# Kernel tuning notes

Measured on AMD Instinct MI355X. Metric: run time of the kernel, lower is better.

The kernel has to match this reference:

```python
import jax, jax.numpy as jnp
import numpy as np

D_NODE = 100
D_HID = 300
EPS = 1e-5


def _gru_step_h0(x, W_ih, b_ih, b_hh):
    # Single torch-GRU step with h0 = 0 (seq len 1), so W_hh @ h0 vanishes
    # and only the hidden biases b_hh survive.
    gi = x @ W_ih.T + b_ih                      # [..., 3*H]
    H = D_HID
    r = jax.nn.sigmoid(gi[..., 0:H] + b_hh[0:H])
    z = jax.nn.sigmoid(gi[..., H:2 * H] + b_hh[H:2 * H])
    n = jnp.tanh(gi[..., 2 * H:3 * H] + r * b_hh[2 * H:3 * H])
    return (1.0 - z) * n                        # h' = (1-z)*n + z*0


def setup_inputs() -> dict:
    key = jax.random.key(0)
    ks = jax.random.split(key, 20)
    B, T, Lq, N = 128, 512, 256, 256
    s = 0.02
    inp = {
        "nodes": jax.random.normal(ks[0], (B * N, D_NODE), jnp.float32),
        "context_rep": jax.random.normal(ks[1], (B, Lq, D_HID), jnp.float32),
        "dia_triples": jax.random.randint(ks[2], (B, T, 3), 0, N, jnp.int64 if jax.config.jax_enable_x64 else jnp.int32),
        "node_number": N,
        # mean_trans: Linear(100, 300)
        "W_mean": s * jax.random.normal(ks[3], (D_HID, D_NODE), jnp.float32),
        "b_mean": jnp.zeros((D_HID,), jnp.float32),
        # bidirectional GRU(300 -> 300); h0=0 so W_hh drops out, keep biases
        "W_ih_f": s * jax.random.normal(ks[4], (3 * D_HID, D_HID), jnp.float32),
        "b_ih_f": s * jax.random.normal(ks[5], (3 * D_HID,), jnp.float32),
        "b_hh_f": s * jax.random.normal(ks[6], (3 * D_HID,), jnp.float32),
        "W_ih_b": s * jax.random.normal(ks[7], (3 * D_HID, D_HID), jnp.float32),
        "b_ih_b": s * jax.random.normal(ks[8], (3 * D_HID,), jnp.float32),
        "b_hh_b": s * jax.random.normal(ks[9], (3 * D_HID,), jnp.float32),
        # output_trans: Linear(600, 300) + tanh
        "W_out": s * jax.random.normal(ks[10], (D_HID, 2 * D_HID), jnp.float32),
        "b_out": jnp.zeros((D_HID,), jnp.float32),
        # trans_node_to_decoder_dim: Linear(100, 300)
        "W_node": s * jax.random.normal(ks[11], (D_HID, D_NODE), jnp.float32),
        "b_node": jnp.zeros((D_HID,), jnp.float32),
        # layernorm(300)
        "gamma": jnp.ones((D_HID,), jnp.float32),
        "beta": jnp.zeros((D_HID,), jnp.float32),
    }
    return inp


def reference(nodes, context_rep, dia_triples, node_number,
              W_mean, b_mean, W_ih_f, b_ih_f, b_hh_f,
              W_ih_b, b_ih_b, b_hh_b, W_out, b_out,
              W_node, b_node, gamma, beta):
    B = context_rep.shape[0]
    N = node_number
    T = dia_triples.shape[1]
    nodes3 = nodes.reshape(B, N, D_NODE)                        # per-dialogue node slices

    # gather head/tail nodes of each triple, mean-aggregate
    head = jnp.broadcast_to(dia_triples[:, :, 0][:, :, None], (B, T, D_NODE))
    tail = jnp.broadcast_to(dia_triples[:, :, -1][:, :, None], (B, T, D_NODE))
    gh = jnp.take_along_axis(nodes3, head, axis=1)              # [B,T,100]
    gt = jnp.take_along_axis(nodes3, tail, axis=1)
    tri_mean = 0.5 * (gh + gt)

    x = tri_mean @ W_mean.T + b_mean                            # [B,T,300] GRU inputs (len-1 paths)

    # bidirectional GRU, one step each direction from h0=0
    h_f = _gru_step_h0(x, W_ih_f, b_ih_f, b_hh_f)
    h_b = _gru_step_h0(x, W_ih_b, b_ih_b, b_hh_b)
    hidden = jnp.concatenate([h_f, h_b], axis=-1)               # [B,T,600]

    hid_ = jnp.tanh(hidden @ W_out.T + b_out)                   # [B,T,300]

    # attention: alpha = softmax(query @ hidden^T, -1).sum(0)
    scores = jnp.einsum("bld,btd->blt", context_rep, hid_)
    alpha = jax.nn.softmax(scores, axis=-1).sum(axis=1)         # [B,T]
    rep = jnp.einsum("bt,btd->bd", alpha, hid_)                 # [B,300]

    mu = rep.mean(axis=-1, keepdims=True)
    var = rep.var(axis=-1, keepdims=True)
    path_feature = (rep - mu) * jax.lax.rsqrt(var + EPS) * gamma + beta
    # dropout is identity in eval mode

    node_feature = nodes3 @ W_node.T + b_node                   # [B,N,300]
    node_mask = jnp.zeros((B, 1, N), dtype=bool)                # equal lengths -> no padding
    return path_feature, node_feature, node_mask
```

## Files before the change

### kernel.cpp

```cpp
#include <hip/hip_runtime.h>
#include <math.h>

#define D_NODE 100
#define D_HID  300
static const int TSEQ = 512, LQn = 256, NNODE = 256;

typedef unsigned int u32;
typedef unsigned short u16;
typedef __attribute__((ext_vector_type(8))) short bf16x8;
typedef __attribute__((ext_vector_type(4))) float f32x4;

__device__ __forceinline__ float bf2f(u16 v){ return __uint_as_float(((u32)v) << 16); }
__device__ __forceinline__ u16 f2bf(float f){
    u32 u = __float_as_uint(f);
    return (u16)((u + 0x7fffu + ((u >> 16) & 1u)) >> 16);
}
__device__ __forceinline__ u32 pack_bf(float lo, float hi){
    return ((u32)f2bf(lo)) | (((u32)f2bf(hi)) << 16);
}
__device__ __forceinline__ void gload_lds16(const void* g, void* l){
    __builtin_amdgcn_global_load_lds(
        (const __attribute__((address_space(1))) u32*)g,
        (__attribute__((address_space(3))) u32*)l, 16, 0, 0);
}
__device__ __forceinline__ float fsig(float x){
    return __builtin_amdgcn_rcpf(1.f + __expf(-x));
}
__device__ __forceinline__ float ftanh(float x){
    return 1.f - 2.f*__builtin_amdgcn_rcpf(1.f + __expf(2.f*x));
}

__global__ __launch_bounds__(128)
void k0_prep(const float* __restrict__ Wm, const float* __restrict__ bm,
             const float* __restrict__ Wihf, const float* __restrict__ bihf, const float* __restrict__ bhhf,
             const float* __restrict__ Wihb, const float* __restrict__ bihb, const float* __restrict__ bhhb,
             u16* __restrict__ W4bf, float* __restrict__ bc, float* __restrict__ bhhn)
{
    int j = blockIdx.x, g = blockIdx.y, dir = blockIdx.z;
    int tid = threadIdx.x;
    u16* wout = W4bf + ((size_t)((dir*3+g)*320 + j))*128;
    if (j >= D_HID) {
        wout[tid] = 0;
        if (tid == 0) { bc[(dir*3+g)*320 + j] = 0.f; if (g==2) bhhn[dir*320+j] = 0.f; }
        return;
    }
    const float* Wih = dir ? Wihb : Wihf;
    const float* bih = dir ? bihb : bihf;
    const float* bhh = dir ? bhhb : bhhf;
    const float* wrow = Wih + (size_t)(g*D_HID + j)*D_HID;
    int k = tid;
    float s = 0.f;
    if (k < D_NODE)
        for (int q = 0; q < D_HID; ++q)
            s = fmaf(wrow[q], Wm[q*D_NODE + k], s);
    wout[k] = f2bf(k < D_NODE ? s : 0.f);

    __shared__ float red[128];
    float p = 0.f;
    for (int q = tid; q < D_HID; q += 128) p = fmaf(bm[q], wrow[q], p);
    red[tid] = p;
    __syncthreads();
    for (int off = 64; off > 0; off >>= 1) {
        if (tid < off) red[tid] += red[tid + off];
        __syncthreads();
    }
    if (tid == 0) {
        float base = bih[g*D_HID + j] + red[0];
        if (g < 2) base += bhh[g*D_HID + j];
        bc[(dir*3+g)*320 + j] = base;
        if (g == 2) bhhn[dir*320 + j] = bhh[2*D_HID + j];
    }
}

__global__ __launch_bounds__(256)
void kW(const float* __restrict__ Wout, const float* __restrict__ Wnode,
        u16* __restrict__ Woutbf, u16* __restrict__ Wnbf)
{
    int idx = blockIdx.x*256 + threadIdx.x;
    if (idx < 320*640) {
        int j = idx / 640, k = idx % 640;
        float v = 0.f;
        if (j < D_HID) {
            if (k < D_HID)                 v = Wout[(size_t)j*600 + k];
            else if (k >= 320 && k < 620)  v = Wout[(size_t)j*600 + (k - 20)];
        }
        Woutbf[idx] = f2bf(v);
    } else {
        int i2 = idx - 320*640;
        if (i2 < 320*128) {
            int j = i2 >> 7, k = i2 & 127;
            float v = (j < D_HID && k < D_NODE) ? Wnode[(size_t)j*D_NODE + k] : 0.f;
            Wnbf[i2] = f2bf(v);
        }
    }
}

__global__ __launch_bounds__(256)
void kA(const float* __restrict__ nodes, const int* __restrict__ trip,
        u32* __restrict__ Abf, u32* __restrict__ Nbf)
{
    int wid  = (blockIdx.x*256 + threadIdx.x) >> 6;
    int nw   = (gridDim.x*256) >> 6;
    int lane = threadIdx.x & 63;
    for (int r = wid; r < 98304; r += nw) {
        if (r < 65536) {
            int b = r >> 9;
            int h  = trip[(size_t)r*3];
            int t2 = trip[(size_t)r*3 + 2];
            const float* nh = nodes + ((size_t)b*NNODE + h)*D_NODE;
            const float* nt = nodes + ((size_t)b*NNODE + t2)*D_NODE;
            u32 v = 0;
            if (lane < 50) {
                float2 a = *(const float2*)(nh + lane*2);
                float2 c = *(const float2*)(nt + lane*2);
                v = pack_bf(0.5f*(a.x + c.x), 0.5f*(a.y + c.y));
            }
            Abf[(size_t)r*64 + lane] = v;
        } else {
            int q = r - 65536;
            u32 v = 0;
            if (lane < 50) {
                float2 a = *(const float2*)(nodes + (size_t)q*D_NODE + lane*2);
                v = pack_bf(a.x, a.y);
            }
            Nbf[(size_t)q*64 + lane] = v;
        }
    }
}

__global__ __launch_bounds__(256)
void kC(const float* __restrict__ ctx, u32* __restrict__ Cbf)
{
    int idx = blockIdx.x*256 + threadIdx.x;
    int r = idx / 40, cp = idx % 40;
    int col = cp*8;
    uint4 v = {0,0,0,0};
    if (col < D_HID) {
        const float* base = ctx + (size_t)r*D_HID + col;
        float4 f0 = *(const float4*)base;
        v.x = pack_bf(f0.x, f0.y); v.y = pack_bf(f0.z, f0.w);
        if (col + 8 <= D_HID) {
            float4 f1 = *(const float4*)(base + 4);
            v.z = pack_bf(f1.x, f1.y); v.w = pack_bf(f1.z, f1.w);
        }
    }
    *(uint4*)(Cbf + (size_t)r*160 + cp*4) = v;
}

__global__ __launch_bounds__(256, 2)
void k1_gru(const u16* __restrict__ Abf, const u16* __restrict__ W4bf,
            const float* __restrict__ bc, const float* __restrict__ bhhn,
            u16* __restrict__ H)
{
    int tid = threadIdx.x;
    int lane = tid & 63, w = tid >> 6;
    int l15 = lane & 15, lq = lane >> 4;
    int m0 = blockIdx.x * 64;

    bf16x8 af[4][4];
    #pragma unroll
    for (int ms = 0; ms < 4; ++ms)
        #pragma unroll
        for (int ks = 0; ks < 4; ++ks)
            af[ms][ks] = *(const bf16x8*)(Abf + ((size_t)(m0 + ms*16 + l15))*128 + ks*32 + lq*8);

    #pragma unroll
    for (int st = 0; st < 10; ++st) {
        const int dir = (st < 5) ? 0 : 1;
        const int jg  = (st < 5) ? st : st - 5;
        const int j0w = jg*64 + w*16;
        const int j = j0w + l15;
        const u16* Wb = W4bf + (size_t)dir*3*320*128;

        bf16x8 bfr[3][4];
        #pragma unroll
        for (int g = 0; g < 3; ++g)
            #pragma unroll
            for (int ks = 0; ks < 4; ++ks)
                bfr[g][ks] = *(const bf16x8*)(Wb + ((size_t)(g*320 + j0w + l15))*128 + ks*32 + lq*8);

        f32x4 acc[4][3];
        #pragma unroll
        for (int ms = 0; ms < 4; ++ms)
            #pragma unroll
            for (int g = 0; g < 3; ++g)
                acc[ms][g] = (f32x4){0.f,0.f,0.f,0.f};

        #pragma unroll
        for (int ms = 0; ms < 4; ++ms)
            #pragma unroll
            for (int ks = 0; ks < 4; ++ks) {
                acc[ms][0] = __builtin_amdgcn_mfma_f32_16x16x32_bf16(af[ms][ks], bfr[0][ks], acc[ms][0], 0,0,0);
                acc[ms][1] = __builtin_amdgcn_mfma_f32_16x16x32_bf16(af[ms][ks], bfr[1][ks], acc[ms][1], 0,0,0);
                acc[ms][2] = __builtin_amdgcn_mfma_f32_16x16x32_bf16(af[ms][ks], bfr[2][ks], acc[ms][2], 0,0,0);
            }

        float bcr = bc[(dir*3+0)*320 + j];
        float bcz = bc[(dir*3+1)*320 + j];
        float bcn = bc[(dir*3+2)*320 + j];
        float bn2 = bhhn[dir*320 + j];
        bool ok = (j < D_HID);
        #pragma unroll
        for (int ms = 0; ms < 4; ++ms)
            #pragma unroll
            for (int i = 0; i < 4; ++i) {
                float r = fsig(acc[ms][0][i] + bcr);
                float z = fsig(acc[ms][1][i] + bcz);
                float n = ftanh(acc[ms][2][i] + bcn + r*bn2);
                float h = (1.f - z)*n;
                H[(size_t)(m0 + ms*16 + lq*4 + i)*640 + dir*320 + j] = ok ? f2bf(h) : (u16)0;
            }
    }
}

__global__ __launch_bounds__(256, 2)
void k2_out(const u16* __restrict__ H, const u16* __restrict__ Woutbf,
            const float* __restrict__ bout, u16* __restrict__ Hid)
{
    __shared__ __attribute__((aligned(16))) char smem[8192];
    int tid = threadIdx.x;
    int lane = tid & 63, w = tid >> 6;
    int l15 = lane & 15, lq = lane >> 4;
    int m0 = blockIdx.x * 64;

    f32x4 acc[4][5];
    #pragma unroll
    for (int ms = 0; ms < 4; ++ms)
        #pragma unroll
        for (int jj = 0; jj < 5; ++jj)
            acc[ms][jj] = (f32x4){0.f,0.f,0.f,0.f};

    for (int c = 0; c < 10; ++c) {
        #pragma unroll
        for (int r = 0; r < 2; ++r) {
            int p = w*2 + r, pm = p >> 1, pk = p & 1;
            gload_lds16(H + ((size_t)(m0 + pm*16 + l15))*640 + c*64 + pk*32 + lq*8,
                        smem + (size_t)(p*64)*16);
        }
        __syncthreads();
        #pragma unroll
        for (int pk = 0; pk < 2; ++pk) {
            bf16x8 bb[5];
            #pragma unroll
            for (int jj = 0; jj < 5; ++jj)
                bb[jj] = *(const bf16x8*)(Woutbf + ((size_t)(w*80 + jj*16 + l15))*640 + c*64 + pk*32 + lq*8);
            #pragma unroll
            for (int ms = 0; ms < 4; ++ms) {
                bf16x8 a = *(const bf16x8*)(smem + (size_t)(((ms*2+pk)*64 + lane))*16);
                #pragma unroll
                for (int jj = 0; jj < 5; ++jj)
                    acc[ms][jj] = __builtin_amdgcn_mfma_f32_16x16x32_bf16(a, bb[jj], acc[ms][jj], 0,0,0);
            }
        }
        __syncthreads();
    }

    #pragma unroll
    for (int jj = 0; jj < 5; ++jj) {
        int j = w*80 + jj*16 + l15;
        bool real = (j < D_HID);
        float bo = real ? bout[j] : 0.f;
        #pragma unroll
        for (int ms = 0; ms < 4; ++ms)
            #pragma unroll
            for (int i = 0; i < 4; ++i) {
                u16 v = real ? f2bf(ftanh(acc[ms][jj][i] + bo)) : (u16)0;
                Hid[(size_t)(m0 + ms*16 + lq*4 + i)*320 + j] = v;
            }
    }
}

__global__ __launch_bounds__(256, 2)
void k3_attn(const u16* __restrict__ Cbf, const u16* __restrict__ Hid,
             float* __restrict__ alphap)
{
    __shared__ char smemA[4096];
    __shared__ char smemB[32768];
    __shared__ float rmax[64*4], rsum[64*4];
    int tid = threadIdx.x;
    int lane = tid & 63, w = tid >> 6;
    int l15 = lane & 15, lq = lane >> 4;
    int id = blockIdx.x;
    int xcd = id & 7, s = id >> 3;
    int bq = s >> 2, mblk = s & 3;
    int b = bq*8 + xcd;
    const u16* Ab = Cbf + ((size_t)b*LQn + mblk*64)*320;
    const u16* Bb = Hid + ((size_t)b*TSEQ)*320;

    f32x4 acc[4][8];
    #pragma unroll
    for (int ms = 0; ms < 4; ++ms)
        #pragma unroll
        for (int g = 0; g < 8; ++g)
            acc[ms][g] = (f32x4){0,0,0,0};

    for (int ks = 0; ks < 10; ++ks) {
        gload_lds16(Ab + ((size_t)(w*16 + l15))*320 + ks*32 + lq*8,
                    smemA + (size_t)(w*64)*16);
        #pragma unroll
        for (int i = 0; i < 8; ++i) {
            int nt = w*8 + i;
            gload_lds16(Bb + ((size_t)(nt*16 + l15))*320 + ks*32 + lq*8,
                        smemB + (size_t)(nt*64)*16);
        }
        __syncthreads();
        bf16x8 afr[4];
        #pragma unroll
        for (int ms = 0; ms < 4; ++ms)
            afr[ms] = *(const bf16x8*)(smemA + (size_t)((ms*64 + lane))*16);
        #pragma unroll
        for (int i = 0; i < 8; ++i) {
            bf16x8 bfr = *(const bf16x8*)(smemB + (size_t)(((w*8+i)*64 + lane))*16);
            #pragma unroll
            for (int ms = 0; ms < 4; ++ms)
                acc[ms][i] = __builtin_amdgcn_mfma_f32_16x16x32_bf16(afr[ms], bfr, acc[ms][i], 0,0,0);
        }
        __syncthreads();
    }

    #pragma unroll
    for (int ms = 0; ms < 4; ++ms)
        #pragma unroll
        for (int i = 0; i < 4; ++i) {
            float m = acc[ms][0][i];
            #pragma unroll
            for (int g = 1; g < 8; ++g) m = fmaxf(m, acc[ms][g][i]);
            m = fmaxf(m, __shfl_xor(m, 1));
            m = fmaxf(m, __shfl_xor(m, 2));
            m = fmaxf(m, __shfl_xor(m, 4));
            m = fmaxf(m, __shfl_xor(m, 8));
            if (l15 == 0) rmax[(ms*16 + lq*4 + i)*4 + w] = m;
        }
    __syncthreads();
    float mfin[4][4];
    #pragma unroll
    for (int ms = 0; ms < 4; ++ms)
        #pragma unroll
        for (int i = 0; i < 4; ++i) {
            float4 mv = *(const float4*)&rmax[(ms*16 + lq*4 + i)*4];
            mfin[ms][i] = fmaxf(fmaxf(mv.x, mv.y), fmaxf(mv.z, mv.w));
        }
    #pragma unroll
    for (int ms = 0; ms < 4; ++ms)
        #pragma unroll
        for (int i = 0; i < 4; ++i) {
            float s2 = 0.f;
            #pragma unroll
            for (int g = 0; g < 8; ++g) {
                float e = __expf(acc[ms][g][i] - mfin[ms][i]);
                acc[ms][g][i] = e;
                s2 += e;
            }
            s2 += __shfl_xor(s2, 1);
            s2 += __shfl_xor(s2, 2);
            s2 += __shfl_xor(s2, 4);
            s2 += __shfl_xor(s2, 8);
            if (l15 == 0) rsum[(ms*16 + lq*4 + i)*4 + w] = s2;
        }
    __syncthreads();
    float inv[4][4];
    #pragma unroll
    for (int ms = 0; ms < 4; ++ms)
        #pragma unroll
        for (int i = 0; i < 4; ++i) {
            float4 sv = *(const float4*)&rsum[(ms*16 + lq*4 + i)*4];
            inv[ms][i] = __builtin_amdgcn_rcpf(sv.x + sv.y + sv.z + sv.w);
        }
    float* ap = alphap + ((size_t)b*4 + mblk)*TSEQ;
    #pragma unroll
    for (int g = 0; g < 8; ++g) {
        float c = 0.f;
        #pragma unroll
        for (int ms = 0; ms < 4; ++ms)
            #pragma unroll
            for (int i = 0; i < 4; ++i)
                c = fmaf(acc[ms][g][i], inv[ms][i], c);
        c += __shfl_xor(c, 16);
        c += __shfl_xor(c, 32);
        if (lq == 0) ap[w*128 + g*16 + l15] = c;
    }
}

__global__ __launch_bounds__(640)
void k4_rep(const float* __restrict__ alphap, const u16* __restrict__ Hid,
            const float* __restrict__ gamma, const float* __restrict__ beta,
            float* __restrict__ outP)
{
    __shared__ float al[512];
    __shared__ float part[320];
    __shared__ float rs[10], rss[10];
    int tid = threadIdx.x, b = blockIdx.x;
    const float* ap = alphap + (size_t)b*4*TSEQ;
    for (int i = tid; i < 512; i += 640)
        al[i] = ap[i] + ap[512 + i] + ap[1024 + i] + ap[1536 + i];
    __syncthreads();
    int half = (tid >= 320) ? 1 : 0;
    int c = tid - half*320;
    float acc = 0.f;
    if (c < D_HID) {
        const u16* hp = Hid + (size_t)b*TSEQ*320 + (size_t)half*256*320 + c;
        float a0 = 0.f, a1 = 0.f;
        #pragma unroll 4
        for (int t = 0; t < 256; t += 2) {
            a0 = fmaf(al[half*256 + t],     bf2f(hp[(size_t)t*320]),       a0);
            a1 = fmaf(al[half*256 + t + 1], bf2f(hp[(size_t)(t+1)*320]),   a1);
        }
        acc = a0 + a1;
    }
    if (half) part[c] = acc;
    __syncthreads();
    float tot = 0.f;
    if (!half) tot = acc + part[c];
    float v = (!half && c < D_HID) ? tot : 0.f;
    float s = v, q = v*v;
    #pragma unroll
    for (int off = 32; off > 0; off >>= 1) { s += __shfl_xor(s, off, 64); q += __shfl_xor(q, off, 64); }
    if ((tid & 63) == 0) { rs[tid >> 6] = s; rss[tid >> 6] = q; }
    __syncthreads();
    float S = rs[0]+rs[1]+rs[2]+rs[3]+rs[4]+rs[5]+rs[6]+rs[7]+rs[8]+rs[9];
    float Q = rss[0]+rss[1]+rss[2]+rss[3]+rss[4]+rss[5]+rss[6]+rss[7]+rss[8]+rss[9];
    float mu = S * (1.f/300.f);
    float var = Q * (1.f/300.f) - mu*mu;
    if (!half && c < D_HID)
        outP[(size_t)b*D_HID + c] = (tot - mu) * rsqrtf(var + 1e-5f) * gamma[c] + beta[c];
}

__global__ __launch_bounds__(256)
void k5_node(const u16* __restrict__ Nbf, const u16* __restrict__ Wnbf,
             const float* __restrict__ bn, float* __restrict__ outN)
{
    __shared__ char smem[16384];
    int tid = threadIdx.x;
    int lane = tid & 63, w = tid >> 6;
    int l15 = lane & 15, lq = lane >> 4;
    int m0 = blockIdx.x * 64;
    int j0w = blockIdx.y*64 + w*16;

    bf16x8 bw[4];
    #pragma unroll
    for (int ks = 0; ks < 4; ++ks)
        bw[ks] = *(const bf16x8*)(Wnbf + ((size_t)(j0w + l15))*128 + ks*32 + lq*8);

    #pragma unroll
    for (int ks = 0; ks < 4; ++ks) {
        const u16* g = Nbf + ((size_t)(m0 + w*16 + l15))*128 + ks*32 + lq*8;
        gload_lds16(g, smem + (size_t)((w*4 + ks)*64)*16);
    }
    __syncthreads();

    f32x4 acc[4];
    #pragma unroll
    for (int ms = 0; ms < 4; ++ms) acc[ms] = (f32x4){0,0,0,0};
    #pragma unroll
    for (int ms = 0; ms < 4; ++ms)
        #pragma unroll
        for (int ks = 0; ks < 4; ++ks) {
            bf16x8 a = *(const bf16x8*)(smem + (size_t)(((ms*4+ks)*64 + lane))*16);
            acc[ms] = __builtin_amdgcn_mfma_f32_16x16x32_bf16(a, bw[ks], acc[ms], 0,0,0);
        }

    int j = j0w + l15;
    if (j < D_HID) {
        float bo = bn[j];
        #pragma unroll
        for (int ms = 0; ms < 4; ++ms)
            #pragma unroll
            for (int i = 0; i < 4; ++i)
                outN[(size_t)(m0 + ms*16 + lq*4 + i)*D_HID + j] = acc[ms][i] + bo;
    }
}

extern "C" void kernel_launch(void* const* d_in, const int* in_sizes, int n_in,
                              void* d_out, int out_size, void* d_ws, size_t ws_size,
                              hipStream_t stream) {
    const float* nodes  = (const float*)d_in[0];
    const float* ctx    = (const float*)d_in[1];
    const int*   trip   = (const int*)d_in[2];
    const float* Wm     = (const float*)d_in[4];
    const float* bm     = (const float*)d_in[5];
    const float* Wihf   = (const float*)d_in[6];
    const float* bihf   = (const float*)d_in[7];
    const float* bhhf   = (const float*)d_in[8];
    const float* Wihb   = (const float*)d_in[9];
    const float* bihb   = (const float*)d_in[10];
    const float* bhhb   = (const float*)d_in[11];
    const float* Wout   = (const float*)d_in[12];
    const float* bout   = (const float*)d_in[13];
    const float* Wnode  = (const float*)d_in[14];
    const float* bnode  = (const float*)d_in[15];
    const float* gamma  = (const float*)d_in[16];
    const float* beta   = (const float*)d_in[17];
    float* out = (float*)d_out;

    char* ws = (char*)d_ws;
    u16*   W4bf   = (u16*)(ws);
    u16*   Woutbf = (u16*)(ws + 491520);
    u16*   Wnbf   = (u16*)(ws + 901120);
    float* bc     = (float*)(ws + 983040);
    float* bhhn   = (float*)(ws + 990720);
    u32*   Abf    = (u32*)(ws + 1048576);
    u32*   Nbf    = (u32*)(ws + 17825792ull);
    u16*   Hhalf  = (u16*)(ws + 26214400ull);
    u32*   Cbf    = (u32*)(ws + 26214400ull);
    u16*   Hid    = (u16*)(ws + 68157440ull);
    float* alphap = (float*)(ws + 110100480ull);

    k0_prep<<<dim3(320,3,2), 128, 0, stream>>>(Wm,bm,Wihf,bihf,bhhf,Wihb,bihb,bhhb,W4bf,bc,bhhn);
    kW     <<<960,  256, 0, stream>>>(Wout,Wnode,Woutbf,Wnbf);
    kA     <<<1024, 256, 0, stream>>>(nodes,trip,Abf,Nbf);

    for (int h = 0; h < 2; ++h) {
        const u16* Ah   = (const u16*)Abf + (size_t)h*32768*128;
        u16*       Hidh = Hid + (size_t)h*32768*320;
        k1_gru<<<512, 256, 0, stream>>>(Ah, W4bf, bc, bhhn, Hhalf);
        k2_out<<<512, 256, 0, stream>>>(Hhalf, Woutbf, bout, Hidh);
    }

    k5_node<<<dim3(512,5), 256, 0, stream>>>((const u16*)Nbf,Wnbf,bnode,out + 38400);
    kC     <<<5120, 256, 0, stream>>>(ctx, Cbf);
    k3_attn<<<512,         256, 0, stream>>>((const u16*)Cbf, Hid, alphap);
    k4_rep <<<128,         640, 0, stream>>>(alphap,Hid,gamma,beta,out);
    hipMemsetAsync(out + 38400 + 9830400, 0, 32768*sizeof(float), stream);
}
```

Measured before the change: 403.3 us.

## Merge prep kernels into one launch and stage GRU A-tile through LDS

The three preprocessing kernels (weight fold, weight bf16 conversion, triple gather) are merged into a single launch that picks its role by block index, removing two launch gaps and letting the independent work run concurrently. The GRU kernel now loads its 64x128 A tile once into LDS with direct global-to-LDS loads, each wave fetching one 16-row slice, then reads its register fragments from LDS. Before, every wave read all four slices straight from global memory. The merged kernel runs the weight-fold blocks at 256 threads with half idle in the dot-product phase, and the GRU kernel gains 16KB of LDS plus a barrier.

```diff
diff --git a/kernel.cpp b/kernel.cpp
--- a/kernel.cpp
+++ b/kernel.cpp
@@ -30,100 +30,102 @@
     return 1.f - 2.f*__builtin_amdgcn_rcpf(1.f + __expf(2.f*x));
 }
 
-__global__ __launch_bounds__(128)
-void k0_prep(const float* __restrict__ Wm, const float* __restrict__ bm,
-             const float* __restrict__ Wihf, const float* __restrict__ bihf, const float* __restrict__ bhhf,
-             const float* __restrict__ Wihb, const float* __restrict__ bihb, const float* __restrict__ bhhb,
-             u16* __restrict__ W4bf, float* __restrict__ bc, float* __restrict__ bhhn)
-{
-    int j = blockIdx.x, g = blockIdx.y, dir = blockIdx.z;
+__global__ __launch_bounds__(256)
+void k_prep(const float* __restrict__ Wout, const float* __restrict__ Wnode,
+            u16* __restrict__ Woutbf, u16* __restrict__ Wnbf,
+            const float* __restrict__ nodes, const int* __restrict__ trip,
+            u32* __restrict__ Abf, u32* __restrict__ Nbf,
+            const float* __restrict__ Wm, const float* __restrict__ bm,
+            const float* __restrict__ Wihf, const float* __restrict__ bihf, const float* __restrict__ bhhf,
+            const float* __restrict__ Wihb, const float* __restrict__ bihb, const float* __restrict__ bhhb,
+            u16* __restrict__ W4bf, float* __restrict__ bc, float* __restrict__ bhhn)
+{
+    __shared__ float red[256];
+    int bid = blockIdx.x;
     int tid = threadIdx.x;
-    u16* wout = W4bf + ((size_t)((dir*3+g)*320 + j))*128;
-    if (j >= D_HID) {
-        wout[tid] = 0;
-        if (tid == 0) { bc[(dir*3+g)*320 + j] = 0.f; if (g==2) bhhn[dir*320+j] = 0.f; }
-        return;
-    }
-    const float* Wih = dir ? Wihb : Wihf;
-    const float* bih = dir ? bihb : bihf;
-    const float* bhh = dir ? bhhb : bhhf;
-    const float* wrow = Wih + (size_t)(g*D_HID + j)*D_HID;
-    int k = tid;
-    float s = 0.f;
-    if (k < D_NODE)
-        for (int q = 0; q < D_HID; ++q)
-            s = fmaf(wrow[q], Wm[q*D_NODE + k], s);
-    wout[k] = f2bf(k < D_NODE ? s : 0.f);
-
-    __shared__ float red[128];
-    float p = 0.f;
-    for (int q = tid; q < D_HID; q += 128) p = fmaf(bm[q], wrow[q], p);
-    red[tid] = p;
-    __syncthreads();
-    for (int off = 64; off > 0; off >>= 1) {
-        if (tid < off) red[tid] += red[tid + off];
+
+    if (bid < 960) {
+        int idx = bid*256 + tid;
+        if (idx < 320*640) {
+            int j = idx / 640, k = idx % 640;
+            float v = 0.f;
+            if (j < D_HID) {
+                if (k < D_HID)                 v = Wout[(size_t)j*600 + k];
+                else if (k >= 320 && k < 620)  v = Wout[(size_t)j*600 + (k - 20)];
+            }
+            Woutbf[idx] = f2bf(v);
+        } else {
+            int i2 = idx - 320*640;
+            if (i2 < 320*128) {
+                int j = i2 >> 7, k = i2 & 127;
+                float v = (j < D_HID && k < D_NODE) ? Wnode[(size_t)j*D_NODE + k] : 0.f;
+                Wnbf[i2] = f2bf(v);
+            }
+        }
+    } else if (bid < 1984) {
+        int wid  = ((bid - 960)*256 + tid) >> 6;
+        const int nw = (1024*256) >> 6;
+        int lane = tid & 63;
+        for (int r = wid; r < 98304; r += nw) {
+            if (r < 65536) {
+                int b = r >> 9;
+                int h  = trip[(size_t)r*3];
+                int t2 = trip[(size_t)r*3 + 2];
+                const float* nh = nodes + ((size_t)b*NNODE + h)*D_NODE;
+                const float* nt = nodes + ((size_t)b*NNODE + t2)*D_NODE;
+                u32 v = 0;
+                if (lane < 50) {
+                    float2 a = *(const float2*)(nh + lane*2);
+                    float2 c = *(const float2*)(nt + lane*2);
+                    v = pack_bf(0.5f*(a.x + c.x), 0.5f*(a.y + c.y));
+                }
+                Abf[(size_t)r*64 + lane] = v;
+            } else {
+                int q = r - 65536;
+                u32 v = 0;
+                if (lane < 50) {
+                    float2 a = *(const float2*)(nodes + (size_t)q*D_NODE + lane*2);
+                    v = pack_bf(a.x, a.y);
+                }
+                Nbf[(size_t)q*64 + lane] = v;
+            }
+        }
+    } else {
+        int lin = bid - 1984;
+        int j   = lin % 320;
+        int g   = (lin / 320) % 3;
+        int dir = lin / 960;
+        u16* wout = W4bf + ((size_t)((dir*3+g)*320 + j))*128;
+        if (j >= D_HID) {
+            if (tid < 128) wout[tid] = 0;
+            if (tid == 0) { bc[(dir*3+g)*320 + j] = 0.f; if (g==2) bhhn[dir*320+j] = 0.f; }
+            return;
+        }
+        const float* Wih = dir ? Wihb : Wihf;
+        const float* bih = dir ? bihb : bihf;
+        const float* bhh = dir ? bhhb : bhhf;
+        const float* wrow = Wih + (size_t)(g*D_HID + j)*D_HID;
+        if (tid < 128) {
+            int k = tid;
+            float s = 0.f;
+            if (k < D_NODE)
+                for (int q = 0; q < D_HID; ++q)
+                    s = fmaf(wrow[q], Wm[q*D_NODE + k], s);
+            wout[k] = f2bf(k < D_NODE ? s : 0.f);
+        }
+        float p = 0.f;
+        for (int q = tid; q < D_HID; q += 256) p = fmaf(bm[q], wrow[q], p);
+        red[tid] = p;
         __syncthreads();
-    }
-    if (tid == 0) {
-        float base = bih[g*D_HID + j] + red[0];
-        if (g < 2) base += bhh[g*D_HID + j];
-        bc[(dir*3+g)*320 + j] = base;
-        if (g == 2) bhhn[dir*320 + j] = bhh[2*D_HID + j];
-    }
-}
-
-__global__ __launch_bounds__(256)
-void kW(const float* __restrict__ Wout, const float* __restrict__ Wnode,
-        u16* __restrict__ Woutbf, u16* __restrict__ Wnbf)
-{
-    int idx = blockIdx.x*256 + threadIdx.x;
-    if (idx < 320*640) {
-        int j = idx / 640, k = idx % 640;
-        float v = 0.f;
-        if (j < D_HID) {
-            if (k < D_HID)                 v = Wout[(size_t)j*600 + k];
-            else if (k >= 320 && k < 620)  v = Wout[(size_t)j*600 + (k - 20)];
-        }
-        Woutbf[idx] = f2bf(v);
-    } else {
-        int i2 = idx - 320*640;
-        if (i2 < 320*128) {
-            int j = i2 >> 7, k = i2 & 127;
-            float v = (j < D_HID && k < D_NODE) ? Wnode[(size_t)j*D_NODE + k] : 0.f;
-            Wnbf[i2] = f2bf(v);
-        }
-    }
-}
-
-__global__ __launch_bounds__(256)
-void kA(const float* __restrict__ nodes, const int* __restrict__ trip,
-        u32* __restrict__ Abf, u32* __restrict__ Nbf)
-{
-    int wid  = (blockIdx.x*256 + threadIdx.x) >> 6;
-    int nw   = (gridDim.x*256) >> 6;
-    int lane = threadIdx.x & 63;
-    for (int r = wid; r < 98304; r += nw) {
-        if (r < 65536) {
-            int b = r >> 9;
-            int h  = trip[(size_t)r*3];
-            int t2 = trip[(size_t)r*3 + 2];
-            const float* nh = nodes + ((size_t)b*NNODE + h)*D_NODE;
-            const float* nt = nodes + ((size_t)b*NNODE + t2)*D_NODE;
-            u32 v = 0;
-            if (lane < 50) {
-                float2 a = *(const float2*)(nh + lane*2);
-                float2 c = *(const float2*)(nt + lane*2);
-                v = pack_bf(0.5f*(a.x + c.x), 0.5f*(a.y + c.y));
-            }
-            Abf[(size_t)r*64 + lane] = v;
-        } else {
-            int q = r - 65536;
-            u32 v = 0;
-            if (lane < 50) {
-                float2 a = *(const float2*)(nodes + (size_t)q*D_NODE + lane*2);
-                v = pack_bf(a.x, a.y);
-            }
-            Nbf[(size_t)q*64 + lane] = v;
+        for (int off = 128; off > 0; off >>= 1) {
+            if (tid < off) red[tid] += red[tid + off];
+            __syncthreads();
+        }
+        if (tid == 0) {
+            float base = bih[g*D_HID + j] + red[0];
+            if (g < 2) base += bhh[g*D_HID + j];
+            bc[(dir*3+g)*320 + j] = base;
+            if (g == 2) bhhn[dir*320 + j] = bhh[2*D_HID + j];
         }
     }
 }
@@ -152,17 +154,25 @@
             const float* __restrict__ bc, const float* __restrict__ bhhn,
             u16* __restrict__ H)
 {
+    __shared__ __attribute__((aligned(16))) char smem[16384];
     int tid = threadIdx.x;
     int lane = tid & 63, w = tid >> 6;
     int l15 = lane & 15, lq = lane >> 4;
     int m0 = blockIdx.x * 64;
 
+    #pragma unroll
+    for (int ks = 0; ks < 4; ++ks) {
+        const u16* g = Abf + ((size_t)(m0 + w*16 + l15))*128 + ks*32 + lq*8;
+        gload_lds16(g, smem + (size_t)((w*4 + ks)*64)*16);
+    }
+    __syncthreads();
+
     bf16x8 af[4][4];
     #pragma unroll
     for (int ms = 0; ms < 4; ++ms)
         #pragma unroll
         for (int ks = 0; ks < 4; ++ks)
-            af[ms][ks] = *(const bf16x8*)(Abf + ((size_t)(m0 + ms*16 + l15))*128 + ks*32 + lq*8);
+            af[ms][ks] = *(const bf16x8*)(smem + (size_t)(((ms*4+ks)*64 + lane))*16);
 
     #pragma unroll
     for (int st = 0; st < 10; ++st) {
@@ -505,9 +515,10 @@
     u16*   Hid    = (u16*)(ws + 68157440ull);
     float* alphap = (float*)(ws + 110100480ull);
 
-    k0_prep<<<dim3(320,3,2), 128, 0, stream>>>(Wm,bm,Wihf,bihf,bhhf,Wihb,bihb,bhhb,W4bf,bc,bhhn);
-    kW     <<<960,  256, 0, stream>>>(Wout,Wnode,Woutbf,Wnbf);
-    kA     <<<1024, 256, 0, stream>>>(nodes,trip,Abf,Nbf);
+    k_prep<<<3904, 256, 0, stream>>>(Wout, Wnode, Woutbf, Wnbf,
+                                     nodes, trip, Abf, Nbf,
+                                     Wm, bm, Wihf, bihf, bhhf, Wihb, bihb, bhhb,
+                                     W4bf, bc, bhhn);
 
     for (int h = 0; h < 2; ++h) {
         const u16* Ah   = (const u16*)Abf + (size_t)h*32768*128;
```

After: 389.0 us. 1.04x faster.
